# Performance work log

Hardware: AMD Instinct MI355X
Metric: run time of the kernel (lower is better)

The kernel has to match this reference:

```python
import jax, jax.numpy as jnp
import numpy as np


def _ds_cumsum(x, d, axis):
    """Discounted cumulative sum y_t = d*y_{t-1} + x_t along `axis`.
    x: [B,C,H,W], d: per-channel discount [C]. Log-depth associative scan."""
    a = jnp.broadcast_to(d[None, :, None, None], x.shape)

    def comb(u, v):
        au, bu = u
        av, bv = v
        return (au * av, bu * av + bv)

    _, y = jax.lax.associative_scan(comb, (a, x), axis=axis)
    return y


def setup_inputs() -> dict:
    key = jax.random.key(0)
    k1, k2, k3 = jax.random.split(key, 3)
    B, C, H, W = 32, 512, 56, 56
    inp = jax.random.normal(k1, (B, C, H, W), dtype=jnp.float32)
    # nn.Linear(C, 2C): weight [2C, C], bias [2C]
    w_proj = jax.random.normal(k2, (2 * C, C), dtype=jnp.float32) * 0.02
    b_proj = jnp.zeros((2 * C,), dtype=jnp.float32)
    # per-channel discount (original init: ones); near-1 values for stability
    discount = jax.random.uniform(k3, (C,), dtype=jnp.float32, minval=0.9, maxval=1.0)
    gamma = jnp.ones((1,), dtype=jnp.float32)
    return {"input": inp, "w_proj": w_proj, "b_proj": b_proj,
            "discount": discount, "gamma": gamma}


def reference(input, w_proj, b_proj, discount, gamma):
    C = input.shape[1]
    # permute->Linear->permute back == channel-dim contraction on NCHW
    x = jnp.einsum('bchw,oc->bohw', input, w_proj) + b_proj[None, :, None, None]
    x_gate = x[:, :C]   # first half: multiplicative branch
    x_scan = x[:, C:]   # second half: scanned branch
    # direction 'nw' (real semiring, discounted): forward scan along H then W
    X_cum = _ds_cumsum(x_scan, discount, axis=2)
    X_cum = _ds_cumsum(X_cum, discount, axis=3)
    gated = x_gate * jax.nn.sigmoid(X_cum)
    return input + gamma * gated
```

## Files before the change

kernel.cpp:

```cpp
#include <hip/hip_runtime.h>
#include <cstddef>
#include <cstdint>

#define BATCH 32
#define CCH   512
#define OCH   1024
#define HW    3136
#define WDIM  56
#define NKT   16

typedef __attribute__((ext_vector_type(8))) short short8v;
typedef __attribute__((ext_vector_type(4))) float f32x4;

static __device__ __forceinline__ unsigned rne2(float x0, float x1) {
    unsigned u0 = __float_as_uint(x0), u1 = __float_as_uint(x1);
    u0 = u0 + 0x7fffu + ((u0 >> 16) & 1u);
    u1 = u1 + 0x7fffu + ((u1 >> 16) & 1u);
    return (u0 >> 16) | (u1 & 0xffff0000u);
}
static __device__ __forceinline__ unsigned short rne1(float x) {
    unsigned u = __float_as_uint(x);
    return (unsigned short)((u + 0x7fffu + ((u >> 16) & 1u)) >> 16);
}
static __device__ __forceinline__ float bf2f(unsigned short h) {
    return __uint_as_float((unsigned)h << 16);
}

static __device__ __forceinline__ int physlot4(int s, int row) {
    return (s ^ (row & 3) ^ ((row >> 2) & 3)) & 3;
}

#define GLD_LDS16(gsrc, ldst) \
    __builtin_amdgcn_global_load_lds( \
        (const __attribute__((address_space(1))) void*)(gsrc), \
        (__attribute__((address_space(3))) void*)(ldst), 16, 0, 0)

#define MFMA16(a, bb, c) __builtin_amdgcn_mfma_f32_16x16x32_bf16((a), (bb), (c), 0, 0, 0)

__global__ __launch_bounds__(256) void preconv_w(
    const float* __restrict__ wp, unsigned char* __restrict__ wcvt)
{
    const int id = blockIdx.x * 256 + threadIdx.x;
    const int o = id >> 4, kt = id & 15;
    const float* p = wp + (size_t)o * CCH + kt * 32;
    unsigned char* dst = wcvt + (size_t)o * 1024 + kt * 64;
    float4 v[8];
#pragma unroll
    for (int r = 0; r < 8; ++r) v[r] = *(const float4*)(p + 4 * r);
#pragma unroll
    for (int oc = 0; oc < 4; ++oc) {
        uint4 w;
        w.x = rne2(v[2*oc].x,   v[2*oc].y);
        w.y = rne2(v[2*oc].z,   v[2*oc].w);
        w.z = rne2(v[2*oc+1].x, v[2*oc+1].y);
        w.w = rne2(v[2*oc+1].z, v[2*oc+1].w);
        *(uint4*)(dst + physlot4(oc, o) * 16) = w;
    }
}

__global__ __launch_bounds__(256) void conv_in(
    const float* __restrict__ in, unsigned char* __restrict__ bin)
{
    const int nt = blockIdx.x;
    const int kt = blockIdx.y;
    const int b  = blockIdx.z;
    const int t  = threadIdx.x;
    __shared__ float sm[32 * 65];

    const int n0 = nt * 64;
    const int row = t >> 3;
    const int c8  = (t & 7) * 8;
    const float* src = in + ((size_t)b * CCH + kt * 32 + row) * HW + n0 + c8;
    float4 v0 = *(const float4*)src;
    float4 v1 = *(const float4*)(src + 4);
    float* sr = sm + row * 65 + c8;
    sr[0] = v0.x; sr[1] = v0.y; sr[2] = v0.z; sr[3] = v0.w;
    sr[4] = v1.x; sr[5] = v1.y; sr[6] = v1.z; sr[7] = v1.w;
    __syncthreads();

    const int n = t >> 2, sub = t & 3;
    const int k0 = sub * 8;
    uint4 w;
    w.x = rne2(sm[(k0 + 0) * 65 + n], sm[(k0 + 1) * 65 + n]);
    w.y = rne2(sm[(k0 + 2) * 65 + n], sm[(k0 + 3) * 65 + n]);
    w.z = rne2(sm[(k0 + 4) * 65 + n], sm[(k0 + 5) * 65 + n]);
    w.w = rne2(sm[(k0 + 6) * 65 + n], sm[(k0 + 7) * 65 + n]);
    *(uint4*)(bin + (((size_t)b * 16 + kt) * HW + n0 + n) * 64 +
              physlot4(sub, n) * 16) = w;
}

template <bool GB>
__global__ __launch_bounds__(256, 4) void gemm_m97(
    const unsigned char* __restrict__ wc,
    const unsigned char* __restrict__ bin,
    const float* __restrict__ bp,
    float* __restrict__ gate,
    unsigned short* __restrict__ gateb,
    unsigned short* __restrict__ scanb)
{
    const int id  = blockIdx.x;
    const int xcd = id & 7;
    const int m   = id >> 3;
    const int ot  = m & 7;
    const int j   = xcd + 8 * (m >> 3);
    const int bx  = j % 25;
    const int b   = j / 25;

    const int t  = threadIdx.x;
    const int lane = t & 63;
    const int wid  = t >> 6;
    const int wm = wid >> 1;
    const int wn = wid & 1;
    const int l15 = lane & 15, lko = lane >> 4;

    __shared__ __align__(16) unsigned char lds[32768];
    unsigned char* const A0 = lds;
    unsigned char* const A1 = lds + 8192;
    unsigned char* const B0 = lds + 16384;
    unsigned char* const B1 = lds + 24576;

    const int o0 = ot * 128;
    const int n0 = bx * 128;

    const unsigned char* aSrc = wc + (size_t)(o0 + (t >> 2)) * 1024 + (t & 3) * 16;
    const unsigned char* bSrc = bin + ((size_t)b * 16 * HW + n0) * 64 + t * 16;

    auto stage = [&](int kt, unsigned char* Ab, unsigned char* Bb) {
#pragma unroll
        for (int jj = 0; jj < 2; ++jj)
            GLD_LDS16(aSrc + kt * 64 + (size_t)(jj * 64) * 1024,
                      Ab + jj * 4096 + wid * 1024);
#pragma unroll
        for (int jj = 0; jj < 2; ++jj)
            GLD_LDS16(bSrc + (size_t)kt * (HW * 64) + jj * 4096,
                      Bb + jj * 4096 + wid * 1024);
    };

    f32x4 acc[4][4] = {};

    auto body = [&](int kt, unsigned char* Ac, unsigned char* Bc,
                    unsigned char* An, unsigned char* Bn) {
        if (kt + 1 < NKT) stage(kt + 1, An, Bn);

        short8v af[4], bf[4];
#pragma unroll
        for (int fi = 0; fi < 4; ++fi) {
            const int r = wm * 64 + fi * 16 + l15;
            af[fi] = *(const short8v*)(Ac + r * 64 + physlot4(lko, r) * 16);
        }
#pragma unroll
        for (int g = 0; g < 4; ++g) {
            const int n = wn * 64 + g * 16 + l15;
            bf[g] = *(const short8v*)(Bc + n * 64 + physlot4(lko, n) * 16);
        }

        __builtin_amdgcn_s_setprio(1);
#pragma unroll
        for (int fi = 0; fi < 4; ++fi)
#pragma unroll
            for (int g = 0; g < 4; ++g)
                acc[fi][g] = MFMA16(af[fi], bf[g], acc[fi][g]);
        __builtin_amdgcn_s_setprio(0);

        asm volatile("s_waitcnt vmcnt(0) lgkmcnt(0)" ::: "memory");
        __builtin_amdgcn_s_barrier();
        asm volatile("" ::: "memory");
    };

    stage(0, A0, B0);
    asm volatile("s_waitcnt vmcnt(0)" ::: "memory");
    __builtin_amdgcn_s_barrier();
    asm volatile("" ::: "memory");

#pragma unroll 1
    for (int kt2 = 0; kt2 < NKT; kt2 += 2) {
        body(kt2,     A0, B0, A1, B1);
        body(kt2 + 1, A1, B1, A0, B0);
    }

    const int c0 = o0 & (CCH - 1);
    if (ot < 4) {
#pragma unroll
        for (int f = 0; f < 4; ++f) {
            const int rowb = wm * 64 + f * 16 + lko * 4;
#pragma unroll
            for (int rg = 0; rg < 4; ++rg) {
                const float bias = bp[o0 + rowb + rg];
                const size_t roff = ((size_t)b * CCH + c0 + rowb + rg) * HW;
#pragma unroll
                for (int g = 0; g < 4; ++g) {
                    const int n = n0 + wn * 64 + g * 16 + l15;
                    if (n < HW) {
                        if constexpr (GB) gateb[roff + n] = rne1(acc[f][g][rg] + bias);
                        else              gate[roff + n]  = acc[f][g][rg] + bias;
                    }
                }
            }
        }
    } else {
#pragma unroll
        for (int f = 0; f < 4; ++f) {
            const int rowb = wm * 64 + f * 16 + lko * 4;
#pragma unroll
            for (int rg = 0; rg < 4; ++rg) {
                const float bias = bp[o0 + rowb + rg];
                unsigned short* drow =
                    scanb + ((size_t)b * CCH + c0 + rowb + rg) * HW;
#pragma unroll
                for (int g = 0; g < 4; ++g) {
                    const int n = n0 + wn * 64 + g * 16 + l15;
                    if (n < HW) drow[n] = rne1(acc[f][g][rg] + bias);
                }
            }
        }
    }
}

__global__ __launch_bounds__(256) void gemm_proj(
    const float* __restrict__ in, const float* __restrict__ wp,
    const float* __restrict__ bp, float* __restrict__ gate,
    float* __restrict__ scan)
{
    const int bx = blockIdx.x, by = blockIdx.y, b = blockIdx.z;
    const int t = threadIdx.x;
    __shared__ float As[16][128];
    __shared__ float Bs[16][64];
    const float* Ab = wp + (size_t)(by * 128) * CCH;
    const float* Bb = in + (size_t)b * CCH * HW + bx * 64;
    float acc[8][4];
#pragma unroll
    for (int i = 0; i < 8; i++)
#pragma unroll
        for (int j = 0; j < 4; j++) acc[i][j] = 0.f;
    const int a_row = t >> 1, a_c = (t & 1) * 8;
    const int b_row = t >> 4, b_n = (t & 15) * 4;
    const int ty = t >> 4, tx = t & 15;
    for (int k0 = 0; k0 < CCH; k0 += 16) {
        float4 av0 = *(const float4*)(Ab + (size_t)a_row * CCH + k0 + a_c);
        float4 av1 = *(const float4*)(Ab + (size_t)a_row * CCH + k0 + a_c + 4);
        float4 bv  = *(const float4*)(Bb + (size_t)(k0 + b_row) * HW + b_n);
        __syncthreads();
        As[a_c + 0][a_row] = av0.x; As[a_c + 1][a_row] = av0.y;
        As[a_c + 2][a_row] = av0.z; As[a_c + 3][a_row] = av0.w;
        As[a_c + 4][a_row] = av1.x; As[a_c + 5][a_row] = av1.y;
        As[a_c + 6][a_row] = av1.z; As[a_c + 7][a_row] = av1.w;
        *(float4*)&Bs[b_row][b_n] = bv;
        __syncthreads();
#pragma unroll
        for (int kk = 0; kk < 16; kk++) {
            float4 a0 = *(const float4*)&As[kk][ty * 8];
            float4 a1 = *(const float4*)&As[kk][ty * 8 + 4];
            float4 bb = *(const float4*)&Bs[kk][tx * 4];
            float av[8] = {a0.x, a0.y, a0.z, a0.w, a1.x, a1.y, a1.z, a1.w};
            float bw[4] = {bb.x, bb.y, bb.z, bb.w};
#pragma unroll
            for (int i = 0; i < 8; i++)
#pragma unroll
                for (int j = 0; j < 4; j++)
                    acc[i][j] = fmaf(av[i], bw[j], acc[i][j]);
        }
    }
    const int n0 = bx * 64 + tx * 4;
#pragma unroll
    for (int i = 0; i < 8; i++) {
        const int o = by * 128 + ty * 8 + i;
        const float bias = bp[o];
        float4 v;
        v.x = acc[i][0] + bias; v.y = acc[i][1] + bias;
        v.z = acc[i][2] + bias; v.w = acc[i][3] + bias;
        float* dst;
        if (o < CCH) dst = gate + ((size_t)b * CCH + o) * HW + n0;
        else         dst = scan + ((size_t)b * CCH + (o - CCH)) * HW + n0;
        *(float4*)dst = v;
    }
}

template <int MODE>
__global__ __launch_bounds__(256) void scan_fuse(
    const float* __restrict__ in,
    const void* __restrict__ scanb_v,
    const void* __restrict__ gate_v,
    const float* __restrict__ disc,
    const float* __restrict__ gamma,
    float* __restrict__ out)
{
    const int idx = blockIdx.x * 4 + (threadIdx.x >> 6);
    const int c = idx & (CCH - 1);
    const size_t base = (size_t)idx * HW;
    const float d = disc[c];
    const float g = gamma[0];
    const int lane = threadIdx.x & 63;
    const int ch4  = threadIdx.x >> 6;

    __shared__ float Lm[4][WDIM * 57];
    float* L = Lm[ch4];

    if (lane < WDIM) {
        const int w = lane;
        float acc = 0.f;
        if constexpr (MODE >= 1) {
            const unsigned short* sb = (const unsigned short*)scanb_v + base;
#pragma unroll 4
            for (int h = 0; h < WDIM; h++) {
                acc = fmaf(d, acc, bf2f(sb[h * WDIM + w]));
                L[h * 57 + w] = acc;
            }
        } else {
            const float* sb = (const float*)scanb_v + base;
#pragma unroll 4
            for (int h = 0; h < WDIM; h++) {
                acc = fmaf(d, acc, sb[h * WDIM + w]);
                L[h * 57 + w] = acc;
            }
        }
    }
    __syncthreads();
    if (lane < WDIM) {
        const int h = lane;
        float acc = 0.f;
#pragma unroll 4
        for (int w = 0; w < WDIM; w++) {
            acc = fmaf(d, acc, L[h * 57 + w]);
            L[h * 57 + w] = acc;
        }
    }
    __syncthreads();
    if (lane < WDIM) {
        const int w = lane;
#pragma unroll 4
        for (int h = 0; h < WDIM; h++) {
            const size_t off = base + h * WDIM + w;
            const float xc = L[h * 57 + w];
            const float sg = 1.f / (1.f + __expf(-xc));
            float gv;
            if constexpr (MODE == 2)
                gv = bf2f(((const unsigned short*)gate_v)[off]);
            else
                gv = ((const float*)gate_v)[off];
            out[off] = fmaf(g * gv, sg, in[off]);
        }
    }
}

extern "C" void kernel_launch(void* const* d_in, const int* in_sizes, int n_in,
                              void* d_out, int out_size, void* d_ws, size_t ws_size,
                              hipStream_t stream) {
    const float* in = (const float*)d_in[0];
    const float* wp = (const float*)d_in[1];
    const float* bp = (const float*)d_in[2];
    const float* dc = (const float*)d_in[3];
    const float* gm = (const float*)d_in[4];
    float* out = (float*)d_out;

    const size_t wcvt_bytes  = (size_t)OCH * CCH * 2;
    const size_t bin_bytes   = (size_t)BATCH * 16 * HW * 64;
    const size_t half_bytes  = (size_t)BATCH * CCH * HW * 2;
    const size_t scan_f32    = (size_t)BATCH * CCH * HW * 4;

    unsigned char*  wcvt  = (unsigned char*)d_ws;
    unsigned char*  bin   = (unsigned char*)d_ws + wcvt_bytes;
    unsigned short* scanb = (unsigned short*)(bin + bin_bytes);
    unsigned short* gateb = (unsigned short*)((unsigned char*)scanb + half_bytes);

    const int nblk = BATCH * CCH / 4;

    if (ws_size >= wcvt_bytes + bin_bytes + 2 * half_bytes) {
        preconv_w<<<64, 256, 0, stream>>>(wp, wcvt);
        conv_in<<<dim3(49, 16, BATCH), 256, 0, stream>>>(in, bin);
        gemm_m97<true><<<6400, 256, 0, stream>>>(wcvt, bin, bp, out, gateb, scanb);
        scan_fuse<2><<<nblk, 256, 0, stream>>>(in, scanb, gateb, dc, gm, out);
    } else if (ws_size >= wcvt_bytes + bin_bytes + half_bytes) {
        preconv_w<<<64, 256, 0, stream>>>(wp, wcvt);
        conv_in<<<dim3(49, 16, BATCH), 256, 0, stream>>>(in, bin);
        gemm_m97<false><<<6400, 256, 0, stream>>>(wcvt, bin, bp, out, nullptr, scanb);
        scan_fuse<1><<<nblk, 256, 0, stream>>>(in, scanb, out, dc, gm, out);
    } else if (ws_size >= scan_f32) {
        float* scanp = (float*)d_ws;
        gemm_proj<<<dim3(HW / 64, OCH / 128, BATCH), 256, 0, stream>>>(
            in, wp, bp, out, scanp);
        scan_fuse<0><<<nblk, 256, 0, stream>>>(in, scanp, out, dc, gm, out);
    }
}
```

Measured before the change: 408.4 us.

## Enlarge GEMM tiles to 256x256 with 8 waves and 4-stage LDS pipeline

Replaces the 128x128-tile, 4-wave double-buffered projection GEMM with a 256x256-tile, 8-wave kernel that uses 128KB of LDS split into four stage buffers. Loads are interleaved across the per-fragment MFMA phases, with fine-grained barriers and vmcnt waits. The aim is more data reuse per loaded byte and better overlap of global-to-LDS transfers with matrix math. In exchange, occupancy drops to one block per CU because of the LDS size, and the grid shrinks to 1664 blocks, so tile waste at the 3136-column edge and tail effects grow.

Result: slower. 432.6 us (+5.9%).

```diff
diff --git a/kernel.cpp b/kernel.cpp
--- a/kernel.cpp
+++ b/kernel.cpp
@@ -90,7 +90,7 @@
 }
 
 template <bool GB>
-__global__ __launch_bounds__(256, 4) void gemm_m97(
+__global__ __launch_bounds__(512, 2) void gemm8p(
     const unsigned char* __restrict__ wc,
     const unsigned char* __restrict__ bin,
     const float* __restrict__ bp,
@@ -101,88 +101,108 @@
     const int id  = blockIdx.x;
     const int xcd = id & 7;
     const int m   = id >> 3;
-    const int ot  = m & 7;
-    const int j   = xcd + 8 * (m >> 3);
-    const int bx  = j % 25;
-    const int b   = j / 25;
+    const int ot  = m & 3;
+    const int j   = xcd + 8 * (m >> 2);
+    const int bx  = j % 13;
+    const int b   = j / 13;
 
     const int t  = threadIdx.x;
     const int lane = t & 63;
     const int wid  = t >> 6;
-    const int wm = wid >> 1;
-    const int wn = wid & 1;
+    const int wm = wid >> 2;
+    const int wn = wid & 3;
     const int l15 = lane & 15, lko = lane >> 4;
 
-    __shared__ __align__(16) unsigned char lds[32768];
-    unsigned char* const A0 = lds;
-    unsigned char* const A1 = lds + 8192;
-    unsigned char* const B0 = lds + 16384;
-    unsigned char* const B1 = lds + 24576;
-
-    const int o0 = ot * 128;
-    const int n0 = bx * 128;
+    __shared__ __align__(16) unsigned char lds[131072];
+    unsigned char* const T0 = lds;
+    unsigned char* const T1 = lds + 32768;
+    unsigned char* const T2 = lds + 65536;
+    unsigned char* const T3 = lds + 98304;
+
+    const int o0 = ot * 256;
+    const int n0 = bx * 256;
 
     const unsigned char* aSrc = wc + (size_t)(o0 + (t >> 2)) * 1024 + (t & 3) * 16;
     const unsigned char* bSrc = bin + ((size_t)b * 16 * HW + n0) * 64 + t * 16;
 
-    auto stage = [&](int kt, unsigned char* Ab, unsigned char* Bb) {
-#pragma unroll
-        for (int jj = 0; jj < 2; ++jj)
-            GLD_LDS16(aSrc + kt * 64 + (size_t)(jj * 64) * 1024,
-                      Ab + jj * 4096 + wid * 1024);
-#pragma unroll
-        for (int jj = 0; jj < 2; ++jj)
-            GLD_LDS16(bSrc + (size_t)kt * (HW * 64) + jj * 4096,
-                      Bb + jj * 4096 + wid * 1024);
+    auto stA = [&](int kt, int jj, unsigned char* buf) {
+        GLD_LDS16(aSrc + (size_t)(jj * 128) * 1024 + kt * 64,
+                  buf + jj * 8192 + wid * 1024);
     };
-
-    f32x4 acc[4][4] = {};
-
-    auto body = [&](int kt, unsigned char* Ac, unsigned char* Bc,
-                    unsigned char* An, unsigned char* Bn) {
-        if (kt + 1 < NKT) stage(kt + 1, An, Bn);
-
-        short8v af[4], bf[4];
-#pragma unroll
-        for (int fi = 0; fi < 4; ++fi) {
-            const int r = wm * 64 + fi * 16 + l15;
-            af[fi] = *(const short8v*)(Ac + r * 64 + physlot4(lko, r) * 16);
-        }
-#pragma unroll
-        for (int g = 0; g < 4; ++g) {
-            const int n = wn * 64 + g * 16 + l15;
-            bf[g] = *(const short8v*)(Bc + n * 64 + physlot4(lko, n) * 16);
-        }
-
-        __builtin_amdgcn_s_setprio(1);
-#pragma unroll
-        for (int fi = 0; fi < 4; ++fi)
-#pragma unroll
-            for (int g = 0; g < 4; ++g)
-                acc[fi][g] = MFMA16(af[fi], bf[g], acc[fi][g]);
-        __builtin_amdgcn_s_setprio(0);
-
-        asm volatile("s_waitcnt vmcnt(0) lgkmcnt(0)" ::: "memory");
-        __builtin_amdgcn_s_barrier();
-        asm volatile("" ::: "memory");
+    auto stB = [&](int kt, int jj, unsigned char* buf) {
+        GLD_LDS16(bSrc + (size_t)kt * (HW * 64) + jj * 8192,
+                  buf + 16384 + jj * 8192 + wid * 1024);
     };
 
-    stage(0, A0, B0);
-    asm volatile("s_waitcnt vmcnt(0)" ::: "memory");
+    f32x4 acc[8][4] = {};
+
+    auto iter = [&](int k0, bool st, unsigned char* Q0, unsigned char* Q1,
+                    unsigned char* S0, unsigned char* S1) {
+        short8v bf[4];
+#pragma unroll
+        for (int p = 0; p < 8; ++p) {
+            unsigned char* buf = (p < 4) ? Q0 : Q1;
+            const int q = p & 3;
+            if (q == 0) {
+#pragma unroll
+                for (int g = 0; g < 4; ++g) {
+                    const int n = wn * 64 + g * 16 + l15;
+                    bf[g] = *(const short8v*)(buf + 16384 + n * 64 +
+                                              physlot4(lko, n) * 16);
+                }
+            }
+            const int r0 = wm * 128 + (2 * q) * 16 + l15;
+            const int r1 = r0 + 16;
+            short8v a0 = *(const short8v*)(buf + r0 * 64 + physlot4(lko, r0) * 16);
+            short8v a1 = *(const short8v*)(buf + r1 * 64 + physlot4(lko, r1) * 16);
+            if (st) {
+                if      (p == 0) stA(k0 + 2, 0, S0);
+                else if (p == 1) stA(k0 + 2, 1, S0);
+                else if (p == 2) stB(k0 + 2, 0, S0);
+                else if (p == 3) stB(k0 + 2, 1, S0);
+                else if (p == 4) stA(k0 + 3, 0, S1);
+                else if (p == 5) stA(k0 + 3, 1, S1);
+                else if (p == 6) stB(k0 + 3, 0, S1);
+                else             stB(k0 + 3, 1, S1);
+            }
+            asm volatile("" ::: "memory");
+            __builtin_amdgcn_s_barrier();
+            asm volatile("" ::: "memory");
+
+            __builtin_amdgcn_s_setprio(1);
+#pragma unroll
+            for (int g = 0; g < 4; ++g) {
+                acc[2 * q][g]     = MFMA16(a0, bf[g], acc[2 * q][g]);
+                acc[2 * q + 1][g] = MFMA16(a1, bf[g], acc[2 * q + 1][g]);
+            }
+            __builtin_amdgcn_s_setprio(0);
+
+            if (p == 3 || p == 7) {
+                if (st) asm volatile("s_waitcnt vmcnt(4)" ::: "memory");
+                else if (p == 3) asm volatile("s_waitcnt vmcnt(0)" ::: "memory");
+            }
+            __builtin_amdgcn_s_barrier();
+            asm volatile("" ::: "memory");
+        }
+    };
+
+    stA(0, 0, T0); stA(0, 1, T0); stB(0, 0, T0); stB(0, 1, T0);
+    stA(1, 0, T1); stA(1, 1, T1); stB(1, 0, T1); stB(1, 1, T1);
+    asm volatile("s_waitcnt vmcnt(4)" ::: "memory");
     __builtin_amdgcn_s_barrier();
     asm volatile("" ::: "memory");
 
 #pragma unroll 1
-    for (int kt2 = 0; kt2 < NKT; kt2 += 2) {
-        body(kt2,     A0, B0, A1, B1);
-        body(kt2 + 1, A1, B1, A0, B0);
+    for (int jj = 0; jj < 4; ++jj) {
+        iter(4 * jj,     true,     T0, T1, T2, T3);
+        iter(4 * jj + 2, jj < 3,   T2, T3, T0, T1);
     }
 
     const int c0 = o0 & (CCH - 1);
-    if (ot < 4) {
-#pragma unroll
-        for (int f = 0; f < 4; ++f) {
-            const int rowb = wm * 64 + f * 16 + lko * 4;
+    if (ot < 2) {
+#pragma unroll
+        for (int f = 0; f < 8; ++f) {
+            const int rowb = wm * 128 + f * 16 + lko * 4;
 #pragma unroll
             for (int rg = 0; rg < 4; ++rg) {
                 const float bias = bp[o0 + rowb + rg];
@@ -199,8 +219,8 @@
         }
     } else {
 #pragma unroll
-        for (int f = 0; f < 4; ++f) {
-            const int rowb = wm * 64 + f * 16 + lko * 4;
+        for (int f = 0; f < 8; ++f) {
+            const int rowb = wm * 128 + f * 16 + lko * 4;
 #pragma unroll
             for (int rg = 0; rg < 4; ++rg) {
                 const float bias = bp[o0 + rowb + rg];
@@ -367,12 +387,12 @@
     if (ws_size >= wcvt_bytes + bin_bytes + 2 * half_bytes) {
         preconv_w<<<64, 256, 0, stream>>>(wp, wcvt);
         conv_in<<<dim3(49, 16, BATCH), 256, 0, stream>>>(in, bin);
-        gemm_m97<true><<<6400, 256, 0, stream>>>(wcvt, bin, bp, out, gateb, scanb);
+        gemm8p<true><<<1664, 512, 0, stream>>>(wcvt, bin, bp, out, gateb, scanb);
         scan_fuse<2><<<nblk, 256, 0, stream>>>(in, scanb, gateb, dc, gm, out);
     } else if (ws_size >= wcvt_bytes + bin_bytes + half_bytes) {
         preconv_w<<<64, 256, 0, stream>>>(wp, wcvt);
         conv_in<<<dim3(49, 16, BATCH), 256, 0, stream>>>(in, bin);
-        gemm_m97<false><<<6400, 256, 0, stream>>>(wcvt, bin, bp, out, nullptr, scanb);
+        gemm8p<false><<<1664, 512, 0, stream>>>(wcvt, bin, bp, out, nullptr, scanb);
         scan_fuse<1><<<nblk, 256, 0, stream>>>(in, scanb, out, dc, gm, out);
     } else if (ws_size >= scan_f32) {
         float* scanp = (float*)d_ws;
```

## Give each wave private LDS tiles to remove block barriers in GEMM loop

Applied to the files above, without the earlier changes.

Each wave now stages its own 64-row A slice and 64-column B slice into a private 16KB LDS region, double buffered. This removes the per-k-step __syncthreads-style barrier, and vmcnt-based waits let loads for step kt+2 overlap compute. The cost is twice the LDS (64KB per block) and duplicated A/B loads across waves, since each wave now loads data that was previously shared. Occupancy drops from 4 to 2 blocks per CU.

Result: slower. 480.1 us (+17.6%).

```diff
diff --git a/kernel.cpp b/kernel.cpp
--- a/kernel.cpp
+++ b/kernel.cpp
@@ -90,7 +90,7 @@
 }
 
 template <bool GB>
-__global__ __launch_bounds__(256, 4) void gemm_m97(
+__global__ __launch_bounds__(256, 2) void gemm_wp(
     const unsigned char* __restrict__ wc,
     const unsigned char* __restrict__ bin,
     const float* __restrict__ bp,
@@ -113,46 +113,58 @@
     const int wn = wid & 1;
     const int l15 = lane & 15, lko = lane >> 4;
 
-    __shared__ __align__(16) unsigned char lds[32768];
-    unsigned char* const A0 = lds;
-    unsigned char* const A1 = lds + 8192;
-    unsigned char* const B0 = lds + 16384;
-    unsigned char* const B1 = lds + 24576;
+    __shared__ __align__(16) unsigned char lds[65536];
+    unsigned char* const wbase = lds + wid * 16384;
 
     const int o0 = ot * 128;
     const int n0 = bx * 128;
 
-    const unsigned char* aSrc = wc + (size_t)(o0 + (t >> 2)) * 1024 + (t & 3) * 16;
-    const unsigned char* bSrc = bin + ((size_t)b * 16 * HW + n0) * 64 + t * 16;
-
-    auto stage = [&](int kt, unsigned char* Ab, unsigned char* Bb) {
-#pragma unroll
-        for (int jj = 0; jj < 2; ++jj)
-            GLD_LDS16(aSrc + kt * 64 + (size_t)(jj * 64) * 1024,
-                      Ab + jj * 4096 + wid * 1024);
-#pragma unroll
-        for (int jj = 0; jj < 2; ++jj)
-            GLD_LDS16(bSrc + (size_t)kt * (HW * 64) + jj * 4096,
-                      Bb + jj * 4096 + wid * 1024);
+    const unsigned char* aSrcW =
+        wc + (size_t)(o0 + wm * 64 + (lane >> 2)) * 1024 + (lane & 3) * 16;
+    const unsigned char* bSrcW =
+        bin + ((size_t)b * 16 * HW + n0 + wn * 64 + (lane >> 2)) * 64 +
+        (lane & 3) * 16;
+
+    auto stage = [&](int kt, int sel) {
+        unsigned char* dst = wbase + sel * 8192;
+#pragma unroll
+        for (int jj = 0; jj < 4; ++jj)
+            GLD_LDS16(aSrcW + (size_t)(jj * 16) * 1024 + kt * 64,
+                      dst + jj * 1024);
+#pragma unroll
+        for (int jj = 0; jj < 4; ++jj)
+            GLD_LDS16(bSrcW + (size_t)kt * (HW * 64) + jj * 1024,
+                      dst + 4096 + jj * 1024);
     };
 
     f32x4 acc[4][4] = {};
 
-    auto body = [&](int kt, unsigned char* Ac, unsigned char* Bc,
-                    unsigned char* An, unsigned char* Bn) {
-        if (kt + 1 < NKT) stage(kt + 1, An, Bn);
+    stage(0, 0);
+    stage(1, 1);
+
+#pragma unroll 1
+    for (int kt = 0; kt < NKT; ++kt) {
+        const int sel = kt & 1;
+        unsigned char* cur = wbase + sel * 8192;
+
+        if (kt + 1 < NKT) asm volatile("s_waitcnt vmcnt(8)" ::: "memory");
+        else              asm volatile("s_waitcnt vmcnt(0)" ::: "memory");
 
         short8v af[4], bf[4];
 #pragma unroll
         for (int fi = 0; fi < 4; ++fi) {
-            const int r = wm * 64 + fi * 16 + l15;
-            af[fi] = *(const short8v*)(Ac + r * 64 + physlot4(lko, r) * 16);
+            const int r = fi * 16 + l15;
+            af[fi] = *(const short8v*)(cur + r * 64 + physlot4(lko, r) * 16);
         }
 #pragma unroll
         for (int g = 0; g < 4; ++g) {
-            const int n = wn * 64 + g * 16 + l15;
-            bf[g] = *(const short8v*)(Bc + n * 64 + physlot4(lko, n) * 16);
-        }
+            const int n = g * 16 + l15;
+            bf[g] = *(const short8v*)(cur + 4096 + n * 64 + physlot4(lko, n) * 16);
+        }
+        asm volatile("s_waitcnt lgkmcnt(0)" ::: "memory");
+        __builtin_amdgcn_sched_barrier(0);
+
+        if (kt + 2 < NKT) stage(kt + 2, sel);
 
         __builtin_amdgcn_s_setprio(1);
 #pragma unroll
@@ -161,21 +173,6 @@
             for (int g = 0; g < 4; ++g)
                 acc[fi][g] = MFMA16(af[fi], bf[g], acc[fi][g]);
         __builtin_amdgcn_s_setprio(0);
-
-        asm volatile("s_waitcnt vmcnt(0) lgkmcnt(0)" ::: "memory");
-        __builtin_amdgcn_s_barrier();
-        asm volatile("" ::: "memory");
-    };
-
-    stage(0, A0, B0);
-    asm volatile("s_waitcnt vmcnt(0)" ::: "memory");
-    __builtin_amdgcn_s_barrier();
-    asm volatile("" ::: "memory");
-
-#pragma unroll 1
-    for (int kt2 = 0; kt2 < NKT; kt2 += 2) {
-        body(kt2,     A0, B0, A1, B1);
-        body(kt2 + 1, A1, B1, A0, B0);
     }
 
     const int c0 = o0 & (CCH - 1);
@@ -367,12 +364,12 @@
     if (ws_size >= wcvt_bytes + bin_bytes + 2 * half_bytes) {
         preconv_w<<<64, 256, 0, stream>>>(wp, wcvt);
         conv_in<<<dim3(49, 16, BATCH), 256, 0, stream>>>(in, bin);
-        gemm_m97<true><<<6400, 256, 0, stream>>>(wcvt, bin, bp, out, gateb, scanb);
+        gemm_wp<true><<<6400, 256, 0, stream>>>(wcvt, bin, bp, out, gateb, scanb);
         scan_fuse<2><<<nblk, 256, 0, stream>>>(in, scanb, gateb, dc, gm, out);
     } else if (ws_size >= wcvt_bytes + bin_bytes + half_bytes) {
         preconv_w<<<64, 256, 0, stream>>>(wp, wcvt);
         conv_in<<<dim3(49, 16, BATCH), 256, 0, stream>>>(in, bin);
-        gemm_m97<false><<<6400, 256, 0, stream>>>(wcvt, bin, bp, out, nullptr, scanb);
+        gemm_wp<false><<<6400, 256, 0, stream>>>(wcvt, bin, bp, out, nullptr, scanb);
         scan_fuse<1><<<nblk, 256, 0, stream>>>(in, scanb, out, dc, gm, out);
     } else if (ws_size >= scan_f32) {
         float* scanp = (float*)d_ws;
```
